# Kernel tuning notes

Hardware: AMD Instinct MI355X
Metric: run time of the kernel (lower is better)

## Reference

```python
import jax, jax.numpy as jnp
import numpy as np

LMAX = 5
RESOLUTION = 12
ASPECT_RATIO = 2
BATCH = 256
NB = 2 * RESOLUTION                       # res_beta = 24
NA = round(2 * ASPECT_RATIO * RESOLUTION)  # res_alpha = res_gamma = 48
DIM = sum((2 * l + 1) ** 2 for l in range(LMAX + 1))  # 286

# normalize2mom constant for tanh: (E_{z~N(0,1)}[tanh(z)^2])^{-1/2}
_x = np.linspace(-12.0, 12.0, 1_000_001)
_pdf = np.exp(-0.5 * _x * _x) / np.sqrt(2.0 * np.pi)
ACT_CST = float(np.trapz(np.tanh(_x) ** 2 * _pdf, _x) ** -0.5)  # ~1.5927


def _su2_generators(j):
    m = np.arange(-j, j)
    raising = np.diag(-np.sqrt(j * (j + 1) - m * (m + 1)), k=-1).astype(complex)
    m = np.arange(-j + 1, j + 1)
    lowering = np.diag(np.sqrt(j * (j + 1) - m * (m - 1)), k=1).astype(complex)
    m = np.arange(-j, j + 1)
    return np.stack([0.5 * (raising + lowering), np.diag(1j * m), -0.5j * (raising - lowering)])


def _q_real_to_complex(l):
    q = np.zeros((2 * l + 1, 2 * l + 1), dtype=complex)
    for m in range(-l, 0):
        q[l + m, l + abs(m)] = 1 / np.sqrt(2)
        q[l + m, l - abs(m)] = -1j / np.sqrt(2)
    q[l, l] = 1
    for m in range(1, l + 1):
        q[l + m, l + abs(m)] = (-1) ** m / np.sqrt(2)
        q[l + m, l - abs(m)] = 1j * (-1) ** m / np.sqrt(2)
    return (-1j) ** l * q


def _so3_generators(l):
    X = _su2_generators(l)
    Q = _q_real_to_complex(l)
    return np.real(np.conj(Q.T)[None] @ X @ Q[None])  # real [3, 2l+1, 2l+1]


def _expm_angles(A, t):
    """exp(t_n * A) for real antisymmetric A via eigendecomposition. -> [n, d, d] real"""
    vals, vecs = np.linalg.eig(A.astype(complex))
    inv = np.linalg.inv(vecs)
    phases = np.exp(t[:, None] * vals[None, :])  # [n, d]
    return np.real(np.einsum('ij,nj,jk->nik', vecs, phases, inv))


def _build_D_and_qw():
    # Euler angle grids (e3nn SO3Grid convention)
    b = (np.arange(NB) + 0.5) / NB * np.pi          # beta   [nb]
    a = np.arange(NA) / NA * 2.0 * np.pi            # alpha=gamma [na]
    blocks = []
    for l in range(LMAX + 1):
        X = _so3_generators(l)
        Ra = _expm_angles(X[1], a)   # exp(alpha * X1)  [na,d,d]
        Rb = _expm_angles(X[0], b)   # exp(beta  * X0)  [nb,d,d]
        # D^l(a,b,c) = Ra[a] @ Rb[b] @ Ra[c]
        Dl = np.einsum('xij,yjk,zkl->xyzil', Ra, Rb, Ra)
        blocks.append(np.sqrt(2 * l + 1) * Dl.reshape(NA, NB, NA, -1))
    D = np.concatenate(blocks, axis=-1).astype(np.float32)  # [na, nb, na, dim]
    # lie_learn / Kostelec-Rockmore quadrature weights for beta
    bb = NB // 2
    k = np.arange(bb)
    j = np.arange(2 * bb)
    w = (2.0 / bb) * np.sin(np.pi * (2 * j + 1) / (4.0 * bb)) * np.sum(
        (1.0 / (2 * k + 1))[None, :]
        * np.sin((2 * j[:, None] + 1) * (2 * k[None, :] + 1) * np.pi / (4.0 * bb)),
        axis=1,
    )
    w = w / (2.0 * (2 * bb) ** 2)
    qw = (w * NB ** 2 / NA ** 2).astype(np.float32)  # [nb]
    return jnp.asarray(D), jnp.asarray(qw)


def setup_inputs() -> dict:
    key = jax.random.key(0)
    features = jax.random.normal(key, (BATCH, DIM), dtype=jnp.float32)
    D, qw = _build_D_and_qw()
    return {"features": features, "D": D, "qw": qw}


def reference(features, D, qw):
    dim = D.shape[-1]
    s = jnp.sqrt(jnp.asarray(dim, features.dtype))
    # to_grid: [B, dim] x [na, nb, na, dim] -> [B, na, nb, na]
    g = jnp.einsum('bi,xyzi->bxyz', features, D) / s
    # normalized pointwise nonlinearity on SO(3) samples
    g = ACT_CST * jnp.tanh(g)
    # from_grid: quadrature-weighted projection back onto flat Wigner basis
    return jnp.einsum('bxyz,y,xyzi->bi', g, qw, D) * s
```

## Files before the change

### kernel.cpp

```cpp
#include <hip/hip_runtime.h>
#include <hip/hip_bf16.h>

#define DIM    286
#define DIMP   288
#define NZTOT  55296
#define NBATCH 256
#define NB_    24
#define NA_    48
#define ZC     32
#define NTILES 1728
#define NCHUNK 192
#define TILES_PER_WG 9
#define S_CONST 16.911534525287763f
#define INV_S   0.05913123959890826f
#define ACT_CST 1.5927f

typedef short bf16x8 __attribute__((ext_vector_type(8)));
typedef float f32x4  __attribute__((ext_vector_type(4)));

#define WS_FBF  0u
#define WS_DBF  147456u
#define WS_DT   (WS_DBF + 31850496u)
#define WS_PART (WS_DT + 31850496u)

typedef const __attribute__((address_space(1))) char GA;
typedef __attribute__((address_space(3))) char LA;
__device__ __forceinline__ void gload_lds16(const void* g, void* l) {
    __builtin_amdgcn_global_load_lds((GA*)g, (LA*)l, 16, 0, 0);
}

__global__ void k_prep(const float* __restrict__ F, const float* __restrict__ D,
                       const float* __restrict__ qw,
                       __hip_bfloat16* __restrict__ Fbf,
                       __hip_bfloat16* __restrict__ Dbf, __hip_bfloat16* __restrict__ Dt2) {
    __shared__ float T[32][305];
    __shared__ float qs[24];
    int t = threadIdx.x;
    int bid = blockIdx.x;
    if (bid >= NTILES) {
        int o = (bid - NTILES) * 256 + t;
        int row = o / DIMP, col = o % DIMP;
        float v = (col < DIM) ? F[row * DIM + col] * INV_S : 0.f;
        Fbf[o] = __float2bfloat16(v);
        return;
    }
    int z0 = bid * 32;
    if (t < 24) qs[t] = qw[t] * S_CONST;
    const float4* Df = (const float4*)(D + (size_t)z0 * DIM);
    for (int k = 0; k < 9; ++k) {
        int idx = t + k * 256;
        if (idx < 2288) {
            float4 v = Df[idx];
            int e = idx * 4;
            int z = e / DIM, i = e % DIM;
            __hip_bfloat162 lo, hi;
            lo.x = __float2bfloat16(v.x); lo.y = __float2bfloat16(v.y);
            hi.x = __float2bfloat16(v.z); hi.y = __float2bfloat16(v.w);
            T[z][i] = v.x; T[z][i + 1] = v.y;
            *(__hip_bfloat162*)(Dbf + (size_t)(z0 + z) * DIMP + i) = lo;
            if (i == 284) {
                T[z + 1][0] = v.z; T[z + 1][1] = v.w;
                *(__hip_bfloat162*)(Dbf + (size_t)(z0 + z + 1) * DIMP) = hi;
            } else {
                T[z][i + 2] = v.z; T[z][i + 3] = v.w;
                *(__hip_bfloat162*)(Dbf + (size_t)(z0 + z) * DIMP + i + 2) = hi;
            }
        }
    }
    if (t < 32) {
        __hip_bfloat162 zz; zz.x = __float2bfloat16(0.f); zz.y = zz.x;
        *(__hip_bfloat162*)(Dbf + (size_t)(z0 + t) * DIMP + DIM) = zz;
    }
    __syncthreads();
    for (int s = 0; s < 5; ++s) {
        int idx = t + s * 256;
        if (idx < 1152) {
            int i = idx >> 2, zc = idx & 3;
            __hip_bfloat16 o8[8];
            #pragma unroll
            for (int j = 0; j < 8; ++j) {
                int zl = zc * 8 + j;
                int y = ((z0 + zl) / NA_) % NB_;
                o8[j] = __float2bfloat16(T[zl][i] * qs[y]);
            }
            *(bf16x8*)(Dt2 + ((size_t)bid * DIMP + i) * ZC + zc * 8) = *(const bf16x8*)o8;
        }
    }
}

__launch_bounds__(256, 2)
__global__ void k_main(const __hip_bfloat16* __restrict__ Fbf,
                       const __hip_bfloat16* __restrict__ Dbf,
                       const __hip_bfloat16* __restrict__ Dt2,
                       __hip_bfloat16* __restrict__ part) {
    __shared__ __align__(16) __hip_bfloat16 Ds[32][288];
    __shared__ __align__(16) __hip_bfloat16 Dts[288][32];
    __shared__ __align__(16) __hip_bfloat16 Gs[4][32][32];

    int t = threadIdx.x;
    int wave = t >> 6, lane = t & 63, ln = lane & 15, q = lane >> 4;

    bf16x8 fa[2][9];
    int rowbase = blockIdx.y * 128 + wave * 32;
    #pragma unroll
    for (int h = 0; h < 2; ++h) {
        const __hip_bfloat16* fp = Fbf + (size_t)(rowbase + h * 16 + ln) * DIMP + q * 8;
        #pragma unroll
        for (int ks = 0; ks < 9; ++ks) fa[h][ks] = *(const bf16x8*)(fp + ks * 32);
    }

    f32x4 acc[2][18];
    #pragma unroll
    for (int h = 0; h < 2; ++h)
        #pragma unroll
        for (int n = 0; n < 18; ++n) acc[h][n] = (f32x4){0.f, 0.f, 0.f, 0.f};

    #pragma unroll 1
    for (int k = 0; k < TILES_PER_WG; ++k) {
        int tz = blockIdx.x + k * NCHUNK;
        {
            const char* src; char* dst;
            if (wave < 2) {
                src = (const char*)(Dbf + (size_t)tz * ZC * DIMP) + wave * 9216 + lane * 16;
                dst = ((char*)&Ds[0][0]) + wave * 9216;
            } else {
                src = (const char*)(Dt2 + (size_t)tz * DIMP * ZC) + (wave - 2) * 9216 + lane * 16;
                dst = ((char*)&Dts[0][0]) + (wave - 2) * 9216;
            }
            #pragma unroll
            for (int j = 0; j < 9; ++j)
                gload_lds16(src + j * 1024, dst + j * 1024);
        }
        asm volatile("s_waitcnt vmcnt(0)" ::: "memory");
        __syncthreads();
        f32x4 g00 = (f32x4){0.f,0.f,0.f,0.f}, g01 = (f32x4){0.f,0.f,0.f,0.f};
        f32x4 g10 = (f32x4){0.f,0.f,0.f,0.f}, g11 = (f32x4){0.f,0.f,0.f,0.f};
        #pragma unroll
        for (int ks = 0; ks < 9; ++ks) {
            bf16x8 b0 = *(const bf16x8*)(&Ds[ln][ks * 32 + q * 8]);
            bf16x8 b1 = *(const bf16x8*)(&Ds[16 + ln][ks * 32 + q * 8]);
            g00 = __builtin_amdgcn_mfma_f32_16x16x32_bf16(fa[0][ks], b0, g00, 0, 0, 0);
            g01 = __builtin_amdgcn_mfma_f32_16x16x32_bf16(fa[0][ks], b1, g01, 0, 0, 0);
            g10 = __builtin_amdgcn_mfma_f32_16x16x32_bf16(fa[1][ks], b0, g10, 0, 0, 0);
            g11 = __builtin_amdgcn_mfma_f32_16x16x32_bf16(fa[1][ks], b1, g11, 0, 0, 0);
        }
        #pragma unroll
        for (int h = 0; h < 2; ++h) {
            #pragma unroll
            for (int zh = 0; zh < 2; ++zh) {
                f32x4 g = (h == 0) ? (zh == 0 ? g00 : g01) : (zh == 0 ? g10 : g11);
                #pragma unroll
                for (int r = 0; r < 4; ++r) {
                    float x = g[r];
                    float a = fabsf(x);
                    float e = __expf(-2.f * a);
                    float th = (1.f - e) / (1.f + e);
                    float v = copysignf(ACT_CST * th, x);
                    Gs[wave][h * 16 + q * 4 + r][zh * 16 + ln] = __float2bfloat16(v);
                }
            }
        }
        bf16x8 a20 = *(const bf16x8*)(&Gs[wave][ln][q * 8]);
        bf16x8 a21 = *(const bf16x8*)(&Gs[wave][16 + ln][q * 8]);
        #pragma unroll
        for (int nf = 0; nf < 18; ++nf) {
            bf16x8 b2 = *(const bf16x8*)(&Dts[nf * 16 + ln][q * 8]);
            acc[0][nf] = __builtin_amdgcn_mfma_f32_16x16x32_bf16(a20, b2, acc[0][nf], 0, 0, 0);
            acc[1][nf] = __builtin_amdgcn_mfma_f32_16x16x32_bf16(a21, b2, acc[1][nf], 0, 0, 0);
        }
        __syncthreads();
    }
    #pragma unroll
    for (int h = 0; h < 2; ++h) {
        __hip_bfloat16* pb = part + ((size_t)blockIdx.x * NBATCH + rowbase + h * 16) * DIMP;
        #pragma unroll
        for (int nf = 0; nf < 18; ++nf) {
            #pragma unroll
            for (int r = 0; r < 4; ++r) {
                pb[(size_t)(q * 4 + r) * DIMP + nf * 16 + ln] = __float2bfloat16(acc[h][nf][r]);
            }
        }
    }
}

__global__ void k_reduce(const __hip_bfloat16* __restrict__ part, float* __restrict__ out) {
    __shared__ float red[3][16][8];
    int t = threadIdx.x, wave = t >> 6, lane = t & 63;
    int j = lane & 15;
    int zg = wave * 4 + (lane >> 4);
    int o8 = blockIdx.x * 16 + j;
    int b = o8 / 36, c8 = o8 % 36;
    const __hip_bfloat16* p = part + (size_t)b * DIMP + c8 * 8;
    float s[8];
    #pragma unroll
    for (int kk = 0; kk < 8; ++kk) s[kk] = 0.f;
    #pragma unroll 4
    for (int ii = 0; ii < 12; ++ii) {
        bf16x8 v = *(const bf16x8*)(p + (size_t)(zg * 12 + ii) * NBATCH * DIMP);
        #pragma unroll
        for (int kk = 0; kk < 8; ++kk) {
            __hip_bfloat16 h; *(short*)&h = v[kk];
            s[kk] += __bfloat162float(h);
        }
    }
    #pragma unroll
    for (int kk = 0; kk < 8; ++kk) {
        s[kk] += __shfl_down(s[kk], 16);
        s[kk] += __shfl_down(s[kk], 32);
    }
    if (wave > 0 && lane < 16) {
        #pragma unroll
        for (int kk = 0; kk < 8; ++kk) red[wave - 1][lane][kk] = s[kk];
    }
    __syncthreads();
    if (wave == 0 && lane < 16) {
        #pragma unroll
        for (int w = 0; w < 3; ++w)
            #pragma unroll
            for (int kk = 0; kk < 8; ++kk) s[kk] += red[w][lane][kk];
        int i0 = c8 * 8;
        #pragma unroll
        for (int kk = 0; kk < 8; ++kk)
            if (i0 + kk < DIM) out[b * DIM + i0 + kk] = s[kk];
    }
}

extern "C" void kernel_launch(void* const* d_in, const int* in_sizes, int n_in,
                              void* d_out, int out_size, void* d_ws, size_t ws_size,
                              hipStream_t stream) {
    const float* F  = (const float*)d_in[0];
    const float* D  = (const float*)d_in[1];
    const float* qw = (const float*)d_in[2];
    char* ws = (char*)d_ws;
    __hip_bfloat16* Fbf = (__hip_bfloat16*)(ws + WS_FBF);
    __hip_bfloat16* Dbf = (__hip_bfloat16*)(ws + WS_DBF);
    __hip_bfloat16* Dt2 = (__hip_bfloat16*)(ws + WS_DT);
    __hip_bfloat16* part = (__hip_bfloat16*)(ws + WS_PART);

    k_prep<<<NTILES + 288, 256, 0, stream>>>(F, D, qw, Fbf, Dbf, Dt2);
    k_main<<<dim3(NCHUNK, 2), 256, 0, stream>>>(Fbf, Dbf, Dt2, part);
    k_reduce<<<576, 256, 0, stream>>>(part, (float*)d_out);
}
```

Measured before the change: 149.1 us.

## Use direct-to-LDS loads in prep and fragment-native layout for partial sums

```diff
diff --git a/kernel.cpp b/kernel.cpp
--- a/kernel.cpp
+++ b/kernel.cpp
@@ -33,7 +33,7 @@
                        const float* __restrict__ qw,
                        __hip_bfloat16* __restrict__ Fbf,
                        __hip_bfloat16* __restrict__ Dbf, __hip_bfloat16* __restrict__ Dt2) {
-    __shared__ float T[32][305];
+    __shared__ __align__(16) float T[9152];
     __shared__ float qs[24];
     int t = threadIdx.x;
     int bid = blockIdx.x;
@@ -46,32 +46,32 @@
     }
     int z0 = bid * 32;
     if (t < 24) qs[t] = qw[t] * S_CONST;
-    const float4* Df = (const float4*)(D + (size_t)z0 * DIM);
-    for (int k = 0; k < 9; ++k) {
-        int idx = t + k * 256;
-        if (idx < 2288) {
-            float4 v = Df[idx];
-            int e = idx * 4;
-            int z = e / DIM, i = e % DIM;
-            __hip_bfloat162 lo, hi;
-            lo.x = __float2bfloat16(v.x); lo.y = __float2bfloat16(v.y);
-            hi.x = __float2bfloat16(v.z); hi.y = __float2bfloat16(v.w);
-            T[z][i] = v.x; T[z][i + 1] = v.y;
-            *(__hip_bfloat162*)(Dbf + (size_t)(z0 + z) * DIMP + i) = lo;
-            if (i == 284) {
-                T[z + 1][0] = v.z; T[z + 1][1] = v.w;
-                *(__hip_bfloat162*)(Dbf + (size_t)(z0 + z + 1) * DIMP) = hi;
-            } else {
-                T[z][i + 2] = v.z; T[z][i + 3] = v.w;
-                *(__hip_bfloat162*)(Dbf + (size_t)(z0 + z) * DIMP + i + 2) = hi;
-            }
-        }
-    }
-    if (t < 32) {
-        __hip_bfloat162 zz; zz.x = __float2bfloat16(0.f); zz.y = zz.x;
-        *(__hip_bfloat162*)(Dbf + (size_t)(z0 + t) * DIMP + DIM) = zz;
-    }
+    {
+        int wave = t >> 6, lane = t & 63;
+        const char* src = (const char*)(D + (size_t)z0 * DIM);
+        char* dst = (char*)T;
+        #pragma unroll
+        for (int j = 0; j < 9; ++j) {
+            int c = wave + j * 4;
+            if (c < 35 || (c == 35 && lane < 48))
+                gload_lds16(src + c * 1024 + lane * 16, dst + c * 1024);
+        }
+    }
+    asm volatile("s_waitcnt vmcnt(0)" ::: "memory");
     __syncthreads();
+    for (int m = 0; m < 18; ++m) {
+        int d = t + m * 256;
+        int z = d / 144, i2 = d % 144;
+        int i = i2 * 2;
+        __hip_bfloat162 o2;
+        if (i < DIM) {
+            float2 v = *(const float2*)(&T[z * DIM + i]);
+            o2.x = __float2bfloat16(v.x); o2.y = __float2bfloat16(v.y);
+        } else {
+            o2.x = __float2bfloat16(0.f); o2.y = o2.x;
+        }
+        *(__hip_bfloat162*)(Dbf + (size_t)(z0 + z) * DIMP + i) = o2;
+    }
     for (int s = 0; s < 5; ++s) {
         int idx = t + s * 256;
         if (idx < 1152) {
@@ -81,7 +81,7 @@
             for (int j = 0; j < 8; ++j) {
                 int zl = zc * 8 + j;
                 int y = ((z0 + zl) / NA_) % NB_;
-                o8[j] = __float2bfloat16(T[zl][i] * qs[y]);
+                o8[j] = __float2bfloat16(T[zl * DIM + i] * qs[y]);
             }
             *(bf16x8*)(Dt2 + ((size_t)bid * DIMP + i) * ZC + zc * 8) = *(const bf16x8*)o8;
         }
@@ -170,15 +170,17 @@
         }
         __syncthreads();
     }
+    __hip_bfloat16* pw = part + (size_t)blockIdx.x * (NBATCH * DIMP)
+                       + ((size_t)blockIdx.y * 128 + wave * 32) * DIMP;
     #pragma unroll
     for (int h = 0; h < 2; ++h) {
-        __hip_bfloat16* pb = part + ((size_t)blockIdx.x * NBATCH + rowbase + h * 16) * DIMP;
-        #pragma unroll
-        for (int nf = 0; nf < 18; ++nf) {
-            #pragma unroll
-            for (int r = 0; r < 4; ++r) {
-                pb[(size_t)(q * 4 + r) * DIMP + nf * 16 + ln] = __float2bfloat16(acc[h][nf][r]);
-            }
+        #pragma unroll
+        for (int m = 0; m < 9; ++m) {
+            __hip_bfloat16 o8[8];
+            #pragma unroll
+            for (int j = 0; j < 8; ++j)
+                o8[j] = __float2bfloat16(acc[h][2 * m + (j >> 2)][j & 3]);
+            *(bf16x8*)(pw + (size_t)((h * 9 + m) * 64 + lane) * 8) = *(const bf16x8*)o8;
         }
     }
 }
@@ -188,40 +190,45 @@
     int t = threadIdx.x, wave = t >> 6, lane = t & 63;
     int j = lane & 15;
     int zg = wave * 4 + (lane >> 4);
-    int o8 = blockIdx.x * 16 + j;
-    int b = o8 / 36, c8 = o8 % 36;
-    const __hip_bfloat16* p = part + (size_t)b * DIMP + c8 * 8;
-    float s[8];
-    #pragma unroll
-    for (int kk = 0; kk < 8; ++kk) s[kk] = 0.f;
+    int s = blockIdx.x * 16 + j;
+    const __hip_bfloat16* p = part + (size_t)s * 8;
+    float sum[8];
+    #pragma unroll
+    for (int kk = 0; kk < 8; ++kk) sum[kk] = 0.f;
     #pragma unroll 4
     for (int ii = 0; ii < 12; ++ii) {
-        bf16x8 v = *(const bf16x8*)(p + (size_t)(zg * 12 + ii) * NBATCH * DIMP);
+        bf16x8 v = *(const bf16x8*)(p + (size_t)(zg * 12 + ii) * (NBATCH * DIMP));
         #pragma unroll
         for (int kk = 0; kk < 8; ++kk) {
             __hip_bfloat16 h; *(short*)&h = v[kk];
-            s[kk] += __bfloat162float(h);
+            sum[kk] += __bfloat162float(h);
         }
     }
     #pragma unroll
     for (int kk = 0; kk < 8; ++kk) {
-        s[kk] += __shfl_down(s[kk], 16);
-        s[kk] += __shfl_down(s[kk], 32);
+        sum[kk] += __shfl_down(sum[kk], 16);
+        sum[kk] += __shfl_down(sum[kk], 32);
     }
     if (wave > 0 && lane < 16) {
         #pragma unroll
-        for (int kk = 0; kk < 8; ++kk) red[wave - 1][lane][kk] = s[kk];
+        for (int kk = 0; kk < 8; ++kk) red[wave - 1][lane][kk] = sum[kk];
     }
     __syncthreads();
     if (wave == 0 && lane < 16) {
         #pragma unroll
         for (int w = 0; w < 3; ++w)
             #pragma unroll
-            for (int kk = 0; kk < 8; ++kk) s[kk] += red[w][lane][kk];
-        int i0 = c8 * 8;
-        #pragma unroll
-        for (int kk = 0; kk < 8; ++kk)
-            if (i0 + kk < DIM) out[b * DIM + i0 + kk] = s[kk];
+            for (int kk = 0; kk < 8; ++kk) sum[kk] += red[w][lane][kk];
+        int wr = s / 1152, si = s % 1152;
+        int lane_m = si % 64, m9 = si / 64;
+        int h = m9 / 9, m = m9 % 9, q = lane_m >> 4, ln = lane_m & 15;
+        int rowb = wr * 32 + h * 16 + q * 4;
+        #pragma unroll
+        for (int j8 = 0; j8 < 8; ++j8) {
+            int nf = 2 * m + (j8 >> 2), r = j8 & 3;
+            int i = nf * 16 + ln;
+            if (i < DIM) out[(rowb + r) * DIM + i] = sum[j8];
+        }
     }
 }
 
```

Result: faster. 142.0 us, median of 2 (-4.8%).
